# Optimization experiments

Measured on AMD Instinct MI355X. Metric: run time of the kernel, lower is better.

## Reference

```python
import jax, jax.numpy as jnp
import numpy as np

T, B, DIN, H, R = 256, 32, 4096, 512, 51
DROP_P = 0.2


def setup_inputs() -> dict:
    key = jax.random.key(0)
    ks = jax.random.split(key, 10)
    x = jax.random.normal(ks[0], (T, B, DIN), jnp.float32)
    # relation id per token; unique within a timestep so the scatter-back
    rel_ids = jax.vmap(lambda k: jax.random.permutation(k, R)[:B])(
        jax.random.split(ks[1], T)).astype(jnp.int32)
    mem_h0 = jnp.zeros((R, H), jnp.float32)  # rel_mem_h, init to 0
    mem_c0 = jnp.zeros((R, H), jnp.float32)  # rel_mem_c, init to 0
    W_in = jax.random.normal(ks[2], (6 * H, DIN), jnp.float32) / np.sqrt(DIN)
    b_in = jnp.zeros((6 * H,), jnp.float32)
    W_state = jax.random.normal(ks[3], (5 * H, H), jnp.float32) / np.sqrt(H)
    # forget-gate bias initialized to 1 (reset_parameters)
    b_state = jnp.zeros((5 * H,), jnp.float32).at[H:2 * H].set(1.0)
    W_out = jax.random.normal(ks[4], (R, H), jnp.float32) / np.sqrt(H)
    b_out = jnp.zeros((R,), jnp.float32)
    keep = jax.random.uniform(ks[5], (B, H)) > DROP_P
    dropout_mask = keep.astype(jnp.float32) / (1.0 - DROP_P)
    return dict(x=x, rel_ids=rel_ids, mem_h0=mem_h0, mem_c0=mem_c0,
                W_in=W_in, b_in=b_in, W_state=W_state, b_state=b_state,
                W_out=W_out, b_out=b_out, dropout_mask=dropout_mask)


def reference(x, rel_ids, mem_h0, mem_c0, W_in, b_in, W_state, b_state,
              W_out, b_out, dropout_mask):
    def step(carry, inp):
        mem_h, mem_c = carry
        x_t, ids = inp                      # (B, DIN), (B,)
        h_prev = mem_h[ids]                 # gather per-relation state (B, H)
        c_prev = mem_c[ids]
        pi = x_t @ W_in.T + b_in            # (B, 6H)
        ps = h_prev @ W_state.T + b_state   # (B, 5H)
        pi_i, pi_f, pi_g, pi_o, pi_hw, pi_proj = jnp.split(pi, 6, axis=-1)
        ps_i, ps_f, ps_g, ps_o, ps_hw = jnp.split(ps, 5, axis=-1)
        i_g = jax.nn.sigmoid(pi_i + ps_i)
        f_g = jax.nn.sigmoid(pi_f + ps_f)
        g = jnp.tanh(pi_g + ps_g)
        o_g = jax.nn.sigmoid(pi_o + ps_o)
        c_new = i_g * g + f_g * c_prev
        h_new = o_g * jnp.tanh(c_new)
        hw = jax.nn.sigmoid(pi_hw + ps_hw)  # highway gate
        h_new = hw * h_new + (1.0 - hw) * pi_proj
        h_new = h_new * dropout_mask        # recurrent dropout (training)
        mem_h = mem_h.at[ids].set(h_new)    # scatter state back per relation
        mem_c = mem_c.at[ids].set(c_new)
        pred = h_new @ W_out.T + b_out      # (B, R)
        return (mem_h, mem_c), pred

    _, preds = jax.lax.scan(step, (mem_h0, mem_c0), (x, rel_ids))
    return preds.reshape(T * B, R)
```

## Files before the change

kernel.cpp:

```cpp
#include <hip/hip_runtime.h>
#include <stdint.h>

#define T_STEPS 256
#define BATCH   32
#define DIN     4096
#define HD      512
#define NREL    51
#define TB      8192
#define SIXH    3072
#define FIVEH   2560
#define SREL    (NREL * HD)
#define PIWG    786432
#define SPIN_MAX (1 << 18)

typedef short bf16x8 __attribute__((ext_vector_type(8)));
typedef float f32x4  __attribute__((ext_vector_type(4)));
typedef unsigned int u32x4 __attribute__((ext_vector_type(4)));

union V16 { u32x4 u; bf16x8 v; };

typedef __attribute__((address_space(1))) const void gvoid_t;
typedef __attribute__((address_space(3))) void lvoid_t;

__device__ inline float bf2f(unsigned short u) {
    return __uint_as_float(((unsigned int)u) << 16);
}
__device__ inline unsigned short f2bf(float f) {
    unsigned int x = __float_as_uint(f);
    x += 0x7fffu + ((x >> 16) & 1u);
    return (unsigned short)(x >> 16);
}
__device__ inline float sigm(float x) {
    return __builtin_amdgcn_rcpf(1.f + __expf(-x));
}
__device__ inline float tanh_fast(float x) {
    return 1.f - 2.f * __builtin_amdgcn_rcpf(1.f + __expf(2.f * x));
}

__device__ inline void gll16(const void* g, void* l) {
    __builtin_amdgcn_global_load_lds((gvoid_t*)g, (lvoid_t*)l, 16, 0, 0);
}

#define GATHER_PLANES(H, L, HP, LP) \
  asm volatile( \
    "global_load_dwordx4 %0, %16, off sc0 sc1\n\t" \
    "global_load_dwordx4 %1, %16, off offset:64 sc0 sc1\n\t" \
    "global_load_dwordx4 %2, %16, off offset:128 sc0 sc1\n\t" \
    "global_load_dwordx4 %3, %16, off offset:192 sc0 sc1\n\t" \
    "global_load_dwordx4 %4, %16, off offset:256 sc0 sc1\n\t" \
    "global_load_dwordx4 %5, %16, off offset:320 sc0 sc1\n\t" \
    "global_load_dwordx4 %6, %16, off offset:384 sc0 sc1\n\t" \
    "global_load_dwordx4 %7, %16, off offset:448 sc0 sc1\n\t" \
    "global_load_dwordx4 %8, %17, off sc0 sc1\n\t" \
    "global_load_dwordx4 %9, %17, off offset:64 sc0 sc1\n\t" \
    "global_load_dwordx4 %10, %17, off offset:128 sc0 sc1\n\t" \
    "global_load_dwordx4 %11, %17, off offset:192 sc0 sc1\n\t" \
    "global_load_dwordx4 %12, %17, off offset:256 sc0 sc1\n\t" \
    "global_load_dwordx4 %13, %17, off offset:320 sc0 sc1\n\t" \
    "global_load_dwordx4 %14, %17, off offset:384 sc0 sc1\n\t" \
    "global_load_dwordx4 %15, %17, off offset:448 sc0 sc1" \
    : "=v"(H[0].u), "=v"(H[1].u), "=v"(H[2].u), "=v"(H[3].u), \
      "=v"(H[4].u), "=v"(H[5].u), "=v"(H[6].u), "=v"(H[7].u), \
      "=v"(L[0].u), "=v"(L[1].u), "=v"(L[2].u), "=v"(L[3].u), \
      "=v"(L[4].u), "=v"(L[5].u), "=v"(L[6].u), "=v"(L[7].u) \
    : "v"(HP), "v"(LP) : "memory")

__device__ inline void coh_store_u16(unsigned short* p, unsigned int v) {
    asm volatile("global_store_short %0, %1, off sc0 sc1" :: "v"(p), "v"(v) : "memory");
}
__device__ inline void coh_store_u32(int* p, int v) {
    asm volatile("global_store_dword %0, %1, off sc0 sc1" :: "v"(p), "v"(v) : "memory");
}
__device__ inline void plain_store_f32(float* p, float v) {
    asm volatile("global_store_dword %0, %1, off" :: "v"(p), "v"(v) : "memory");
}

__global__ void k_cvt(const float* __restrict__ s, unsigned short* __restrict__ d, int n4) {
    int i = blockIdx.x * blockDim.x + threadIdx.x;
    int st = gridDim.x * blockDim.x;
    for (; i < n4; i += st) {
        float4 v = ((const float4*)s)[i];
        ushort4 o;
        o.x = f2bf(v.x); o.y = f2bf(v.y); o.z = f2bf(v.z); o.w = f2bf(v.w);
        ((ushort4*)d)[i] = o;
    }
}

__global__ void k_zero(int* __restrict__ p) {
    int i = blockIdx.x * blockDim.x + threadIdx.x;
    if (i < 2048) p[i] = 0;
}

__global__ __launch_bounds__(256) void k_gemm_pi(const unsigned short* __restrict__ xb,
                                                 const unsigned short* __restrict__ wb,
                                                 const float* __restrict__ bin,
                                                 unsigned short* __restrict__ PI2) {
    __shared__ unsigned short sA[128 * 32];
    __shared__ unsigned short sB[128 * 32];
    const int tid = threadIdx.x;
    const int w = tid >> 6, l = tid & 63;
    const int wr = w >> 1, wc = w & 1;
    const long brow = (long)blockIdx.y * 128;
    const long bcol = (long)blockIdx.x * 128;

    f32x4 acc[4][4] = {};

    const int c0 = w * 128 + l;
    const int r0 = c0 >> 2, kc0 = (c0 & 3) * 8;
    const int c1 = c0 + 64;
    const int r1 = c1 >> 2, kc1 = (c1 & 3) * 8;
    unsigned short* lds0A = sA + (w * 128) * 8;
    unsigned short* lds1A = sA + (w * 128 + 64) * 8;
    unsigned short* lds0B = sB + (w * 128) * 8;
    unsigned short* lds1B = sB + (w * 128 + 64) * 8;

    const int frow = l & 15, kg = (l >> 4) * 8;

    for (int k0 = 0; k0 < DIN; k0 += 32) {
        __syncthreads();
        gll16(xb + (brow + r0) * DIN + k0 + kc0, lds0A);
        gll16(xb + (brow + r1) * DIN + k0 + kc1, lds1A);
        gll16(wb + (bcol + r0) * DIN + k0 + kc0, lds0B);
        gll16(wb + (bcol + r1) * DIN + k0 + kc1, lds1B);
        __syncthreads();
        bf16x8 aF[4], bF[4];
#pragma unroll
        for (int m = 0; m < 4; ++m)
            aF[m] = *(const bf16x8*)(sA + (wr * 64 + m * 16 + frow) * 32 + kg);
#pragma unroll
        for (int n = 0; n < 4; ++n)
            bF[n] = *(const bf16x8*)(sB + (wc * 64 + n * 16 + frow) * 32 + kg);
#pragma unroll
        for (int m = 0; m < 4; ++m)
#pragma unroll
            for (int n = 0; n < 4; ++n)
                acc[m][n] = __builtin_amdgcn_mfma_f32_16x16x32_bf16(aF[m], bF[n], acc[m][n], 0, 0, 0);
    }

#pragma unroll
    for (int m = 0; m < 4; ++m) {
#pragma unroll
        for (int n = 0; n < 4; ++n) {
            const long col = bcol + wc * 64 + n * 16 + (l & 15);
            const float bv = bin[col];
            const int g = (int)(col >> 9);
            const int cc = (int)(col & 511);
            const size_t base = (size_t)(cc >> 4) * PIWG + (size_t)(g * 16 + (cc & 15));
#pragma unroll
            for (int r = 0; r < 4; ++r) {
                const long row = brow + wr * 64 + m * 16 + (l >> 4) * 4 + r;
                PI2[base + (size_t)row * 96] = f2bf(acc[m][n][r] + bv);
            }
        }
    }
}

__global__ __launch_bounds__(256, 1) void k_recur(
    const int* __restrict__ rel, const float* __restrict__ h0,
    const float* __restrict__ c0, const unsigned short* __restrict__ PI2,
    const unsigned short* __restrict__ wsb,
    const float* __restrict__ bst, const float* __restrict__ drop,
    unsigned short* __restrict__ Hp, int* __restrict__ ctr, float* __restrict__ Hs)
{
    __shared__ unsigned short piB[2][4096];
    __shared__ unsigned char relS[T_STEPS * BATCH];
    __shared__ unsigned long long pref[T_STEPS];
    __shared__ float cS[NREL * 16];
    __shared__ float red[2][2][5][256];
    __shared__ float pad1[4096];
    __shared__ float pad2[1024];

    const int tid = threadIdx.x;
    const int w = tid >> 6, l = tid & 63;
    const int slot = blockIdx.x;
    const int hc0 = slot * 16;
    const unsigned short* slabBase = PI2 + (size_t)slot * PIWG;
    unsigned short* HpL = Hp + 2 * SREL;
    int* myflag = ctr + slot * 32;

    for (int i = tid; i < T_STEPS * BATCH; i += 256) relS[i] = (unsigned char)rel[i];
    __syncthreads();
    if (relS[0] == 255) { pad1[tid] = 1.f; pad2[tid & 1023] = pad1[255 - tid]; cS[0] = pad2[0]; }

    {
        unsigned long long f = 0;
        for (int b = 0; b < BATCH; ++b) f ^= 1ull << relS[tid * BATCH + b];
        pref[tid] = f;
    }
    __syncthreads();
    if (tid == 0) {
        unsigned long long run = 0;
        for (int t = 0; t < T_STEPS; ++t) {
            const unsigned long long f = pref[t];
            pref[t] = run;
            run ^= f;
        }
    }

    const int m = w & 1, kh = w >> 1;
    const int frow = l & 15, koff = l >> 4;
    const int col = hc0 + frow;

    bf16x8 Wr[5][8];
#pragma unroll
    for (int g = 0; g < 5; ++g)
#pragma unroll
        for (int kk = 0; kk < 8; ++kk)
            Wr[g][kk] = *(const bf16x8*)(wsb + (size_t)(g * HD + hc0 + frow) * HD
                                         + kh * 256 + kk * 32 + koff * 8);

    for (int i = tid; i < NREL * 16; i += 256) {
        const int r = i >> 4, c = hc0 + (i & 15);
        cS[i] = c0[r * HD + c];
        const float hv = h0[r * HD + c];
        const unsigned short hi = f2bf(hv);
        coh_store_u16(Hp + r * HD + c, hi);
        coh_store_u16(HpL + r * HD + c, (unsigned int)f2bf(hv - bf2f(hi)));
    }

    gll16(slabBase + (w * 64 + l) * 8, &piB[0][0] + (w * 64 + l) * 8);
    gll16(slabBase + (256 + w * 64 + l) * 8, &piB[0][0] + (256 + w * 64 + l) * 8);

    float bs0 = bst[col], bs1 = bst[HD + col], bs2 = bst[2 * HD + col];
    float bs3 = bst[3 * HD + col], bs4 = bst[4 * HD + col];
    const int rA = kh * 2, rB = rA + 1;
    const int bA = m * 16 + (l >> 4) * 4 + rA;
    const int bB = bA + 1;
    const float dropA = drop[bA * HD + col];
    const float dropB = drop[bB * HD + col];

    __syncthreads();
    asm volatile("s_waitcnt vmcnt(0)" ::: "memory");
    __builtin_amdgcn_s_barrier();
    if (tid == 64) coh_store_u32(myflag, 1);
    if (w == 0) {
        const int* fp = ctr + ((l < 32) ? l : 31) * 32;
        int fv, it = 0;
        do {
            asm volatile("global_load_dword %0, %1, off sc0 sc1\n\ts_waitcnt vmcnt(0)"
                         : "=v"(fv) : "v"(fp) : "memory");
        } while (!__all(fv >= 1) && ++it < SPIN_MAX);
    }
    __syncthreads();

    for (int t = 0; t < T_STEPS; ++t) {
        const unsigned long long pm = pref[t];

        const int id = relS[t * BATCH + m * 16 + frow];
        const unsigned short* hp = Hp + (int)((pm >> id) & 1) * SREL + id * HD + kh * 256 + koff * 8;
        const unsigned short* lp = hp + 2 * SREL;
        V16 hF[8], lF[8];
        GATHER_PLANES(hF, lF, hp, lp);
        asm volatile("s_waitcnt vmcnt(8)" ::: "memory");
        __builtin_amdgcn_sched_barrier(0);

        f32x4 acch[5] = {}, accl[5] = {};
#pragma unroll
        for (int kk = 0; kk < 8; ++kk)
#pragma unroll
            for (int g = 0; g < 5; ++g)
                acch[g] = __builtin_amdgcn_mfma_f32_16x16x32_bf16(hF[kk].v, Wr[g][kk], acch[g], 0, 0, 0);

        asm volatile("s_waitcnt vmcnt(0)" ::: "memory");
        __builtin_amdgcn_sched_barrier(0);

#pragma unroll
        for (int kk = 0; kk < 8; ++kk)
#pragma unroll
            for (int g = 0; g < 5; ++g)
                accl[g] = __builtin_amdgcn_mfma_f32_16x16x32_bf16(lF[kk].v, Wr[g][kk], accl[g], 0, 0, 0);

        f32x4 own[5];
#pragma unroll
        for (int g = 0; g < 5; ++g) {
            own[g] = acch[g] + accl[g];
            *(f32x4*)&red[m][kh][g][l * 4] = own[g];
        }
        __syncthreads();

        float hOutA, hOutB;
        int bAr, bBr;
        {
            float psA[5], psB[5];
#pragma unroll
            for (int g = 0; g < 5; ++g) {
                const f32x4 oth = *(const f32x4*)&red[m][kh ^ 1][g][l * 4];
                psA[g] = own[g][rA] + oth[rA];
                psB[g] = own[g][rB] + oth[rB];
            }
            const unsigned short* pb = &piB[t & 1][0];
            const unsigned short* prA = pb + bA * 96 + frow;
            const unsigned short* prB = pb + bB * 96 + frow;
            const int idA = relS[t * BATCH + bA];
            const int idB = relS[t * BATCH + bB];
            bAr = idA; bBr = idB;
            {
                const float ig = sigm(bf2f(prA[0])  + psA[0] + bs0);
                const float fg = sigm(bf2f(prA[16]) + psA[1] + bs1);
                const float gg = tanh_fast(bf2f(prA[32]) + psA[2] + bs2);
                const float og = sigm(bf2f(prA[48]) + psA[3] + bs3);
                const float hw = sigm(bf2f(prA[64]) + psA[4] + bs4);
                const float cp = cS[idA * 16 + frow];
                const float cn = ig * gg + fg * cp;
                float h = og * tanh_fast(cn);
                h = hw * h + (1.f - hw) * bf2f(prA[80]);
                h *= dropA;
                cS[idA * 16 + frow] = cn;
                hOutA = h;
            }
            {
                const float ig = sigm(bf2f(prB[0])  + psB[0] + bs0);
                const float fg = sigm(bf2f(prB[16]) + psB[1] + bs1);
                const float gg = tanh_fast(bf2f(prB[32]) + psB[2] + bs2);
                const float og = sigm(bf2f(prB[48]) + psB[3] + bs3);
                const float hw = sigm(bf2f(prB[64]) + psB[4] + bs4);
                const float cp = cS[idB * 16 + frow];
                const float cn = ig * gg + fg * cp;
                float h = og * tanh_fast(cn);
                h = hw * h + (1.f - hw) * bf2f(prB[80]);
                h *= dropB;
                cS[idB * 16 + frow] = cn;
                hOutB = h;
            }
        }

        {
            const unsigned short hhiA = f2bf(hOutA);
            const unsigned short hloA = f2bf(hOutA - bf2f(hhiA));
            const unsigned short hhiB = f2bf(hOutB);
            const unsigned short hloB = f2bf(hOutB - bf2f(hhiB));
            const int pwA = (int)(((pm >> bAr) & 1) ^ 1ull);
            const int pwB = (int)(((pm >> bBr) & 1) ^ 1ull);
            coh_store_u16(Hp + pwA * SREL + bAr * HD + col, hhiA);
            coh_store_u16(HpL + pwA * SREL + bAr * HD + col, hloA);
            coh_store_u16(Hp + pwB * SREL + bBr * HD + col, hhiB);
            coh_store_u16(HpL + pwB * SREL + bBr * HD + col, hloB);
            plain_store_f32(Hs + (size_t)(t * BATCH + bA) * HD + col, hOutA);
            plain_store_f32(Hs + (size_t)(t * BATCH + bB) * HD + col, hOutB);
            __builtin_amdgcn_sched_barrier(0);
            const int tn = (t + 1 < T_STEPS) ? (t + 1) : 0;
            const unsigned short* gsl = slabBase + (size_t)tn * 3072;
            unsigned short* dst = &piB[tn & 1][0];
            gll16(gsl + (w * 64 + l) * 8, dst + (w * 64 + l) * 8);
            gll16(gsl + (256 + w * 64 + l) * 8, dst + (256 + w * 64 + l) * 8);
            __builtin_amdgcn_sched_barrier(0);
        }

        asm volatile("s_waitcnt vmcnt(4)" ::: "memory");
        __builtin_amdgcn_sched_barrier(0);
        __builtin_amdgcn_s_barrier();

        if (tid == 64) coh_store_u32(myflag, t + 2);
        if (w == 0) {
            const int* fp = ctr + ((l < 32) ? l : 31) * 32;
            int fv, it = 0;
            do {
                asm volatile("global_load_dword %0, %1, off sc0 sc1\n\ts_waitcnt vmcnt(0)"
                             : "=v"(fv) : "v"(fp) : "memory");
            } while (!__all(fv >= t + 2) && ++it < SPIN_MAX);
        }
        __syncthreads();
    }
}

__global__ __launch_bounds__(256) void k_pred(const float* __restrict__ Hs,
                                              const float* __restrict__ Wout,
                                              const float* __restrict__ bout,
                                              float* __restrict__ out) {
    __shared__ float hT[16 * HD];
    const int tid = threadIdx.x;
    const long row0 = (long)blockIdx.x * 16;
    for (int i = tid; i < (16 * HD) / 4; i += 256)
        ((float4*)hT)[i] = ((const float4*)(Hs + row0 * HD))[i];
    __syncthreads();
    const int w = tid >> 6, c = tid & 63;
    if (c < NREL) {
        float a0 = bout[c], a1 = a0, a2 = a0, a3 = a0;
        const float* wrp = Wout + c * HD;
        for (int k = 0; k < HD; k += 4) {
            const float4 wv = *(const float4*)(wrp + k);
            const float4 h0 = *(const float4*)(hT + (w * 4 + 0) * HD + k);
            const float4 h1 = *(const float4*)(hT + (w * 4 + 1) * HD + k);
            const float4 h2 = *(const float4*)(hT + (w * 4 + 2) * HD + k);
            const float4 h3 = *(const float4*)(hT + (w * 4 + 3) * HD + k);
            a0 += wv.x * h0.x + wv.y * h0.y + wv.z * h0.z + wv.w * h0.w;
            a1 += wv.x * h1.x + wv.y * h1.y + wv.z * h1.z + wv.w * h1.w;
            a2 += wv.x * h2.x + wv.y * h2.y + wv.z * h2.z + wv.w * h2.w;
            a3 += wv.x * h3.x + wv.y * h3.y + wv.z * h3.z + wv.w * h3.w;
        }
        out[(row0 + w * 4 + 0) * NREL + c] = a0;
        out[(row0 + w * 4 + 1) * NREL + c] = a1;
        out[(row0 + w * 4 + 2) * NREL + c] = a2;
        out[(row0 + w * 4 + 3) * NREL + c] = a3;
    }
}

extern "C" void kernel_launch(void* const* d_in, const int* in_sizes, int n_in,
                              void* d_out, int out_size, void* d_ws, size_t ws_size,
                              hipStream_t stream) {
    const float* x    = (const float*)d_in[0];
    const int*   rel  = (const int*)  d_in[1];
    const float* h0   = (const float*)d_in[2];
    const float* c0   = (const float*)d_in[3];
    const float* Win  = (const float*)d_in[4];
    const float* bin  = (const float*)d_in[5];
    const float* Wst  = (const float*)d_in[6];
    const float* bst  = (const float*)d_in[7];
    const float* Wout = (const float*)d_in[8];
    const float* bout = (const float*)d_in[9];
    const float* drop = (const float*)d_in[10];

    char* ws = (char*)d_ws;
    unsigned short* xb  = (unsigned short*)(ws);
    unsigned short* wb  = (unsigned short*)(ws + 67108864);
    unsigned short* wsb = (unsigned short*)(ws + 92274688);
    unsigned short* PI2 = (unsigned short*)(ws + 94896128);
    unsigned short* Hp  = (unsigned short*)(ws + 145227776);
    float*          Hs  = (float*)         (ws + 145436672);
    int*            ctr = (int*)           (ws + 162213888);
    float* out = (float*)d_out;

    k_zero<<<8, 256, 0, stream>>>(ctr);
    k_cvt<<<2048, 256, 0, stream>>>(x, xb, (TB * DIN) / 4);
    k_cvt<<<1024, 256, 0, stream>>>(Win, wb, (SIXH * DIN) / 4);
    k_cvt<<<320, 256, 0, stream>>>(Wst, wsb, (FIVEH * HD) / 4);

    k_gemm_pi<<<dim3(SIXH / 128, TB / 128), 256, 0, stream>>>(xb, wb, bin, PI2);

    k_recur<<<32, 256, 0, stream>>>(rel, h0, c0, PI2, wsb, bst, drop, Hp, ctr, Hs);

    k_pred<<<512, 256, 0, stream>>>(Hs, Wout, bout, out);
}
```

Baseline: 1.611 ms.

## Fuse input GEMM and recurrence into one persistent kernel with per-row-block readiness flags

```diff
diff --git a/kernel.cpp b/kernel.cpp
--- a/kernel.cpp
+++ b/kernel.cpp
@@ -11,6 +11,8 @@
 #define FIVEH   2560
 #define SREL    (NREL * HD)
 #define PIWG    786432
+#define NTILES  1536
+#define GWGS    224
 #define SPIN_MAX (1 << 18)
 
 typedef short bf16x8 __attribute__((ext_vector_type(8)));
@@ -74,6 +76,12 @@
 __device__ inline void plain_store_f32(float* p, float v) {
     asm volatile("global_store_dword %0, %1, off" :: "v"(p), "v"(v) : "memory");
 }
+__device__ inline int coh_load_i32(const int* p) {
+    int v;
+    asm volatile("global_load_dword %0, %1, off sc0 sc1\n\ts_waitcnt vmcnt(0)"
+                 : "=v"(v) : "v"(p) : "memory");
+    return v;
+}
 
 __global__ void k_cvt(const float* __restrict__ s, unsigned short* __restrict__ d, int n4) {
     int i = blockIdx.x * blockDim.x + threadIdx.x;
@@ -91,96 +99,109 @@
     if (i < 2048) p[i] = 0;
 }
 
-__global__ __launch_bounds__(256) void k_gemm_pi(const unsigned short* __restrict__ xb,
-                                                 const unsigned short* __restrict__ wb,
-                                                 const float* __restrict__ bin,
-                                                 unsigned short* __restrict__ PI2) {
-    __shared__ unsigned short sA[128 * 32];
-    __shared__ unsigned short sB[128 * 32];
+__global__ __launch_bounds__(256, 1) void k_main(
+    const int* __restrict__ rel, const float* __restrict__ h0,
+    const float* __restrict__ c0, unsigned short* __restrict__ PI2,
+    const unsigned short* __restrict__ wsb,
+    const float* __restrict__ bst, const float* __restrict__ drop,
+    unsigned short* __restrict__ Hp, int* __restrict__ ctr, float* __restrict__ Hs,
+    const unsigned short* __restrict__ xb, const unsigned short* __restrict__ wb,
+    const float* __restrict__ bin)
+{
+    __shared__ union {
+        struct {
+            unsigned short piB[2][8192];
+            unsigned char  relS[T_STEPS * BATCH];
+            unsigned long long pref[T_STEPS];
+            float cS[NREL * 16];
+            float red[2][2][5][256];
+        } r;
+        struct {
+            unsigned short sA[128 * 32];
+            unsigned short sB[128 * 32];
+        } g;
+    } sm;
+
     const int tid = threadIdx.x;
     const int w = tid >> 6, l = tid & 63;
-    const int wr = w >> 1, wc = w & 1;
-    const long brow = (long)blockIdx.y * 128;
-    const long bcol = (long)blockIdx.x * 128;
-
-    f32x4 acc[4][4] = {};
-
-    const int c0 = w * 128 + l;
-    const int r0 = c0 >> 2, kc0 = (c0 & 3) * 8;
-    const int c1 = c0 + 64;
-    const int r1 = c1 >> 2, kc1 = (c1 & 3) * 8;
-    unsigned short* lds0A = sA + (w * 128) * 8;
-    unsigned short* lds1A = sA + (w * 128 + 64) * 8;
-    unsigned short* lds0B = sB + (w * 128) * 8;
-    unsigned short* lds1B = sB + (w * 128 + 64) * 8;
-
-    const int frow = l & 15, kg = (l >> 4) * 8;
-
-    for (int k0 = 0; k0 < DIN; k0 += 32) {
-        __syncthreads();
-        gll16(xb + (brow + r0) * DIN + k0 + kc0, lds0A);
-        gll16(xb + (brow + r1) * DIN + k0 + kc1, lds1A);
-        gll16(wb + (bcol + r0) * DIN + k0 + kc0, lds0B);
-        gll16(wb + (bcol + r1) * DIN + k0 + kc1, lds1B);
-        __syncthreads();
-        bf16x8 aF[4], bF[4];
-#pragma unroll
-        for (int m = 0; m < 4; ++m)
-            aF[m] = *(const bf16x8*)(sA + (wr * 64 + m * 16 + frow) * 32 + kg);
-#pragma unroll
-        for (int n = 0; n < 4; ++n)
-            bF[n] = *(const bf16x8*)(sB + (wc * 64 + n * 16 + frow) * 32 + kg);
-#pragma unroll
-        for (int m = 0; m < 4; ++m)
-#pragma unroll
-            for (int n = 0; n < 4; ++n)
-                acc[m][n] = __builtin_amdgcn_mfma_f32_16x16x32_bf16(aF[m], bF[n], acc[m][n], 0, 0, 0);
-    }
-
-#pragma unroll
-    for (int m = 0; m < 4; ++m) {
-#pragma unroll
-        for (int n = 0; n < 4; ++n) {
-            const long col = bcol + wc * 64 + n * 16 + (l & 15);
-            const float bv = bin[col];
-            const int g = (int)(col >> 9);
-            const int cc = (int)(col & 511);
-            const size_t base = (size_t)(cc >> 4) * PIWG + (size_t)(g * 16 + (cc & 15));
-#pragma unroll
-            for (int r = 0; r < 4; ++r) {
-                const long row = brow + wr * 64 + m * 16 + (l >> 4) * 4 + r;
-                PI2[base + (size_t)row * 96] = f2bf(acc[m][n][r] + bv);
-            }
-        }
-    }
-}
-
-__global__ __launch_bounds__(256, 1) void k_recur(
-    const int* __restrict__ rel, const float* __restrict__ h0,
-    const float* __restrict__ c0, const unsigned short* __restrict__ PI2,
-    const unsigned short* __restrict__ wsb,
-    const float* __restrict__ bst, const float* __restrict__ drop,
-    unsigned short* __restrict__ Hp, int* __restrict__ ctr, float* __restrict__ Hs)
-{
-    __shared__ unsigned short piB[2][4096];
-    __shared__ unsigned char relS[T_STEPS * BATCH];
-    __shared__ unsigned long long pref[T_STEPS];
-    __shared__ float cS[NREL * 16];
-    __shared__ float red[2][2][5][256];
-    __shared__ float pad1[4096];
-    __shared__ float pad2[1024];
-
-    const int tid = threadIdx.x;
-    const int w = tid >> 6, l = tid & 63;
+    int* done = ctr + 1024;
+
+    if (blockIdx.x >= 32) {
+        const int gbid = blockIdx.x - 32;
+        const int wr = w >> 1, wc = w & 1;
+        const int frow = l & 15, kg = (l >> 4) * 8;
+        const int c0i = w * 128 + l;
+        const int r0 = c0i >> 2, kc0 = (c0i & 3) * 8;
+        const int c1i = c0i + 64;
+        const int r1 = c1i >> 2, kc1 = (c1i & 3) * 8;
+        unsigned short* lds0A = sm.g.sA + (w * 128) * 8;
+        unsigned short* lds1A = sm.g.sA + (w * 128 + 64) * 8;
+        unsigned short* lds0B = sm.g.sB + (w * 128) * 8;
+        unsigned short* lds1B = sm.g.sB + (w * 128 + 64) * 8;
+
+        for (int i = gbid; i < NTILES; i += GWGS) {
+            const int by = i / 24, bx = i % 24;
+            const long brow = (long)by * 128;
+            const long bcol = (long)bx * 128;
+
+            f32x4 acc[4][4] = {};
+            for (int k0 = 0; k0 < DIN; k0 += 32) {
+                __syncthreads();
+                gll16(xb + (brow + r0) * DIN + k0 + kc0, lds0A);
+                gll16(xb + (brow + r1) * DIN + k0 + kc1, lds1A);
+                gll16(wb + (bcol + r0) * DIN + k0 + kc0, lds0B);
+                gll16(wb + (bcol + r1) * DIN + k0 + kc1, lds1B);
+                __syncthreads();
+                bf16x8 aF[4], bF[4];
+#pragma unroll
+                for (int mm = 0; mm < 4; ++mm)
+                    aF[mm] = *(const bf16x8*)(sm.g.sA + (wr * 64 + mm * 16 + frow) * 32 + kg);
+#pragma unroll
+                for (int nn = 0; nn < 4; ++nn)
+                    bF[nn] = *(const bf16x8*)(sm.g.sB + (wc * 64 + nn * 16 + frow) * 32 + kg);
+#pragma unroll
+                for (int mm = 0; mm < 4; ++mm)
+#pragma unroll
+                    for (int nn = 0; nn < 4; ++nn)
+                        acc[mm][nn] = __builtin_amdgcn_mfma_f32_16x16x32_bf16(aF[mm], bF[nn], acc[mm][nn], 0, 0, 0);
+            }
+
+#pragma unroll
+            for (int mm = 0; mm < 4; ++mm) {
+#pragma unroll
+                for (int nn = 0; nn < 4; ++nn) {
+                    const long col = bcol + wc * 64 + nn * 16 + (l & 15);
+                    const float bv = bin[col];
+                    const int g2 = (int)(col >> 9);
+                    const int cc = (int)(col & 511);
+                    const size_t base = (size_t)(cc >> 4) * PIWG + (size_t)(g2 * 16 + (cc & 15));
+#pragma unroll
+                    for (int r = 0; r < 4; ++r) {
+                        const long row = brow + wr * 64 + mm * 16 + (l >> 4) * 4 + r;
+                        coh_store_u16(PI2 + base + (size_t)row * 96,
+                                      (unsigned int)f2bf(acc[mm][nn][r] + bv));
+                    }
+                }
+            }
+            asm volatile("s_waitcnt vmcnt(0)" ::: "memory");
+            __syncthreads();
+            if (tid == 0) atomicAdd(&done[by], 1);
+        }
+        return;
+    }
+
     const int slot = blockIdx.x;
     const int hc0 = slot * 16;
     const unsigned short* slabBase = PI2 + (size_t)slot * PIWG;
     unsigned short* HpL = Hp + 2 * SREL;
     int* myflag = ctr + slot * 32;
 
+    unsigned char* relS = sm.r.relS;
+    unsigned long long* pref = sm.r.pref;
+    float* cS = sm.r.cS;
+
     for (int i = tid; i < T_STEPS * BATCH; i += 256) relS[i] = (unsigned char)rel[i];
     __syncthreads();
-    if (relS[0] == 255) { pad1[tid] = 1.f; pad2[tid & 1023] = pad1[255 - tid]; cS[0] = pad2[0]; }
 
     {
         unsigned long long f = 0;
@@ -218,8 +239,14 @@
         coh_store_u16(HpL + r * HD + c, (unsigned int)f2bf(hv - bf2f(hi)));
     }
 
-    gll16(slabBase + (w * 64 + l) * 8, &piB[0][0] + (w * 64 + l) * 8);
-    gll16(slabBase + (256 + w * 64 + l) * 8, &piB[0][0] + (256 + w * 64 + l) * 8);
+    int readyUpto;
+    {
+        int dv, it = 0;
+        do { dv = coh_load_i32(done + 0); } while (dv < 24 && ++it < SPIN_MAX);
+        readyUpto = 1;
+    }
+    gll16(slabBase + (w * 64 + l) * 8, &sm.r.piB[0][0] + (w * 64 + l) * 8);
+    gll16(slabBase + (256 + w * 64 + l) * 8, &sm.r.piB[0][0] + (256 + w * 64 + l) * 8);
 
     float bs0 = bst[col], bs1 = bst[HD + col], bs2 = bst[2 * HD + col];
     float bs3 = bst[3 * HD + col], bs4 = bst[4 * HD + col];
@@ -236,10 +263,7 @@
     if (w == 0) {
         const int* fp = ctr + ((l < 32) ? l : 31) * 32;
         int fv, it = 0;
-        do {
-            asm volatile("global_load_dword %0, %1, off sc0 sc1\n\ts_waitcnt vmcnt(0)"
-                         : "=v"(fv) : "v"(fp) : "memory");
-        } while (!__all(fv >= 1) && ++it < SPIN_MAX);
+        do { fv = coh_load_i32(fp); } while (!__all(fv >= 1) && ++it < SPIN_MAX);
     }
     __syncthreads();
 
@@ -274,7 +298,7 @@
 #pragma unroll
         for (int g = 0; g < 5; ++g) {
             own[g] = acch[g] + accl[g];
-            *(f32x4*)&red[m][kh][g][l * 4] = own[g];
+            *(f32x4*)&sm.r.red[m][kh][g][l * 4] = own[g];
         }
         __syncthreads();
 
@@ -284,11 +308,11 @@
             float psA[5], psB[5];
 #pragma unroll
             for (int g = 0; g < 5; ++g) {
-                const f32x4 oth = *(const f32x4*)&red[m][kh ^ 1][g][l * 4];
+                const f32x4 oth = *(const f32x4*)&sm.r.red[m][kh ^ 1][g][l * 4];
                 psA[g] = own[g][rA] + oth[rA];
                 psB[g] = own[g][rB] + oth[rB];
             }
-            const unsigned short* pb = &piB[t & 1][0];
+            const unsigned short* pb = &sm.r.piB[t & 1][0];
             const unsigned short* prA = pb + bA * 96 + frow;
             const unsigned short* prB = pb + bB * 96 + frow;
             const int idA = relS[t * BATCH + bA];
@@ -338,9 +362,23 @@
             plain_store_f32(Hs + (size_t)(t * BATCH + bA) * HD + col, hOutA);
             plain_store_f32(Hs + (size_t)(t * BATCH + bB) * HD + col, hOutB);
             __builtin_amdgcn_sched_barrier(0);
+
+            if (t + 1 < T_STEPS && readyUpto < 64) {
+                const int rb = (t + 1) >> 2;
+                if (rb >= readyUpto) {
+                    int dv = coh_load_i32(done + 63);
+                    if (dv >= 24) readyUpto = 64;
+                    else {
+                        int it = 0;
+                        do { dv = coh_load_i32(done + rb); } while (dv < 24 && ++it < SPIN_MAX);
+                        readyUpto = rb + 1;
+                    }
+                }
+            }
+
             const int tn = (t + 1 < T_STEPS) ? (t + 1) : 0;
             const unsigned short* gsl = slabBase + (size_t)tn * 3072;
-            unsigned short* dst = &piB[tn & 1][0];
+            unsigned short* dst = &sm.r.piB[tn & 1][0];
             gll16(gsl + (w * 64 + l) * 8, dst + (w * 64 + l) * 8);
             gll16(gsl + (256 + w * 64 + l) * 8, dst + (256 + w * 64 + l) * 8);
             __builtin_amdgcn_sched_barrier(0);
@@ -354,10 +392,7 @@
         if (w == 0) {
             const int* fp = ctr + ((l < 32) ? l : 31) * 32;
             int fv, it = 0;
-            do {
-                asm volatile("global_load_dword %0, %1, off sc0 sc1\n\ts_waitcnt vmcnt(0)"
-                             : "=v"(fv) : "v"(fp) : "memory");
-            } while (!__all(fv >= t + 2) && ++it < SPIN_MAX);
+            do { fv = coh_load_i32(fp); } while (!__all(fv >= t + 2) && ++it < SPIN_MAX);
         }
         __syncthreads();
     }
@@ -425,9 +460,8 @@
     k_cvt<<<1024, 256, 0, stream>>>(Win, wb, (SIXH * DIN) / 4);
     k_cvt<<<320, 256, 0, stream>>>(Wst, wsb, (FIVEH * HD) / 4);
 
-    k_gemm_pi<<<dim3(SIXH / 128, TB / 128), 256, 0, stream>>>(xb, wb, bin, PI2);
-
-    k_recur<<<32, 256, 0, stream>>>(rel, h0, c0, PI2, wsb, bst, drop, Hp, ctr, Hs);
+    k_main<<<256, 256, 0, stream>>>(rel, h0, c0, PI2, wsb, bst, drop, Hp, ctr, Hs,
+                                    xb, wb, bin);
 
     k_pred<<<512, 256, 0, stream>>>(Hs, Wout, bout, out);
 }
```

Measured after the change: 1.558 ms. 3.3% less time.
